# Kernel optimization log

Hardware: AMD Instinct MI355X
Metric: run time of the kernel (lower is better)

Reference implementation:

```python
import jax, jax.numpy as jnp
import numpy as np

N = 50000      # nodes
E = 500000     # edges (includes N self-loops)
DIN = 512
DOUT = 256
NEG_SLOPE = 0.01  # torch nn.LeakyReLU default


def setup_inputs() -> dict:
    key = jax.random.key(0)
    k1, k2, k3, k4, k5 = jax.random.split(key, 5)
    x = jax.random.normal(k1, (N, DIN), dtype=jnp.float32)
    # xavier_normal_ with gain=1.414
    std_W = 1.414 * np.sqrt(2.0 / (DIN + DOUT))
    W = jax.random.normal(k2, (DIN, DOUT), dtype=jnp.float32) * std_W
    std_a = 1.414 * np.sqrt(2.0 / (1 + 2 * DOUT))
    a = jax.random.normal(k3, (2 * DOUT,), dtype=jnp.float32) * std_a
    # first N edges are self-loops so every row-sum is nonzero
    loops = jnp.arange(N, dtype=jnp.int32)
    edge_src = jnp.concatenate([loops, jax.random.randint(k4, (E - N,), 0, N, dtype=jnp.int32)])
    edge_dst = jnp.concatenate([loops, jax.random.randint(k5, (E - N,), 0, N, dtype=jnp.int32)])
    return {"x": x, "W": W, "a": a, "edge_src": edge_src, "edge_dst": edge_dst}


def reference(x, W, a, edge_src, edge_dst):
    n = x.shape[0]
    d = W.shape[1]
    h = x @ W  # [N, DOUT]
    # a . [h_src ; h_dst] decomposed per-node, then gathered per-edge
    s_src = h @ a[:d]   # [N]
    s_dst = h @ a[d:]   # [N]
    score = s_src[edge_src] + s_dst[edge_dst]          # [E]
    e = jnp.exp(-jax.nn.leaky_relu(score, NEG_SLOPE))  # [E]
    # sparse softmax denominator: spmm(edge, e, ones) == segment sum over src
    e_rowsum = jax.ops.segment_sum(e, edge_src, num_segments=n)            # [N]
    # numerator: spmm(edge, e, h) == sum_j e_ij * h_j per row i
    h_prime = jax.ops.segment_sum(e[:, None] * h[edge_dst], edge_src, num_segments=n)  # [N, DOUT]
    h_prime = h_prime / e_rowsum[:, None]
    return jax.nn.elu(h_prime)  # concat=True branch
```

## Files before the change

### kernel.cpp

```cpp
#include <hip/hip_runtime.h>
#include <math.h>

#define DIN 512
#define DOUT 256
#define NEG_SLOPE 0.01f

typedef __attribute__((ext_vector_type(8))) short bf16x8;
typedef __attribute__((ext_vector_type(4))) float f32x4;
typedef __attribute__((ext_vector_type(4))) unsigned int u32x4;

__device__ __forceinline__ unsigned short f2bf(float f) {
    unsigned int u = __float_as_uint(f);
    unsigned int r = (u + 0x7FFFu + ((u >> 16) & 1u)) >> 16;
    return (unsigned short)r;
}
__device__ __forceinline__ float bf2f(unsigned short u) {
    return __uint_as_float(((unsigned int)u) << 16);
}
__device__ __forceinline__ unsigned int cvtpk(float lo, float hi) {
    unsigned int r;
    asm("v_cvt_pk_bf16_f32 %0, %1, %2" : "=v"(r) : "v"(lo), "v"(hi));
    return r;
}
__device__ __forceinline__ void gload16(const void* g, void* l) {
    __builtin_amdgcn_global_load_lds(
        (const __attribute__((address_space(1))) void*)g,
        (__attribute__((address_space(3))) void*)l, 16, 0, 0);
}

__global__ void prep(const float* __restrict__ W, unsigned short* __restrict__ Bp,
                     int* __restrict__ deg, float* __restrict__ s_src,
                     float* __restrict__ s_dst, int N) {
    int t = blockIdx.x * blockDim.x + threadIdx.x;
    if (t < (DIN / 32) * (DOUT / 16) * 64) {
        int lane = t & 63;
        int cg = (t >> 6) & 15;
        int ks = t >> 10;
        int l15 = lane & 15, g = lane >> 4;
        int col = cg * 16 + l15;
        int k0 = ks * 32 + g * 8;
        ushort4 lo, hi;
        lo.x = f2bf(W[(size_t)(k0 + 0) * DOUT + col]);
        lo.y = f2bf(W[(size_t)(k0 + 1) * DOUT + col]);
        lo.z = f2bf(W[(size_t)(k0 + 2) * DOUT + col]);
        lo.w = f2bf(W[(size_t)(k0 + 3) * DOUT + col]);
        hi.x = f2bf(W[(size_t)(k0 + 4) * DOUT + col]);
        hi.y = f2bf(W[(size_t)(k0 + 5) * DOUT + col]);
        hi.z = f2bf(W[(size_t)(k0 + 6) * DOUT + col]);
        hi.w = f2bf(W[(size_t)(k0 + 7) * DOUT + col]);
        *(ushort4*)(Bp + (size_t)t * 8) = lo;
        *(ushort4*)(Bp + (size_t)t * 8 + 4) = hi;
    }
    if (t < N) { deg[t] = 0; s_src[t] = 0.f; s_dst[t] = 0.f; }
}

__global__ __launch_bounds__(64, 3) void gemm_k(const float* __restrict__ x,
                                                const unsigned short* __restrict__ Bp,
                                                unsigned short* __restrict__ hb,
                                                const float* __restrict__ av,
                                                float* __restrict__ s_src,
                                                float* __restrict__ s_dst, int M) {
    __shared__ unsigned char As[16384];
    const int lane = threadIdx.x;
    const int l15 = lane & 15;
    const int g = lane >> 4;
    const int m0 = blockIdx.x * 32;
    const int half = blockIdx.y;

    auto stage = [&](int bb, int ks) {
#pragma unroll
        for (int it = 0; it < 4; ++it) {
            int s = it * 64 + lane;
            int row = s >> 3;
            int slot = s & 7;
            int q = slot ^ (row & 7);
            int rg = min(m0 + row, M - 1);
            const float* src = x + (size_t)rg * DIN + ks * 32 + q * 4;
            gload16(src, As + bb * 4096 + it * 1024);
        }
    };

    const unsigned short* pB = Bp + ((size_t)(half * 8) * 64 + lane) * 8;
    f32x4 acc[2][8] = {};
    bf16x8 bB[2][8];

    stage(0, 0);
    stage(1, 1);
#pragma unroll
    for (int cg = 0; cg < 8; ++cg)
        bB[0][cg] = *(const bf16x8*)(pB + (size_t)cg * 512);

#pragma unroll
    for (int ks = 0; ks < 16; ++ks) {
        if (ks < 14) stage((ks + 2) & 3, ks + 2);
        if (ks < 15) {
            const unsigned short* pBn = pB + (size_t)(ks + 1) * 16 * 512;
#pragma unroll
            for (int cg = 0; cg < 8; ++cg)
                bB[(ks + 1) & 1][cg] = *(const bf16x8*)(pBn + (size_t)cg * 512);
        }
        __builtin_amdgcn_sched_barrier(0);
        if (ks < 14)      asm volatile("s_waitcnt vmcnt(24)");
        else if (ks == 14) asm volatile("s_waitcnt vmcnt(20)");
        else               asm volatile("s_waitcnt vmcnt(16)");
        __builtin_amdgcn_sched_barrier(0);
        const unsigned char* Ab = As + (ks & 3) * 4096;
        const int rr0 = l15, rr1 = l15 + 16;
        f32x4 v0 = *(const f32x4*)(Ab + rr0 * 128 + (((2 * g) ^ (rr0 & 7)) << 4));
        f32x4 v1 = *(const f32x4*)(Ab + rr0 * 128 + (((2 * g + 1) ^ (rr0 & 7)) << 4));
        f32x4 w0 = *(const f32x4*)(Ab + rr1 * 128 + (((2 * g) ^ (rr1 & 7)) << 4));
        f32x4 w1 = *(const f32x4*)(Ab + rr1 * 128 + (((2 * g + 1) ^ (rr1 & 7)) << 4));
        u32x4 p;
        p.x = cvtpk(v0.x, v0.y); p.y = cvtpk(v0.z, v0.w);
        p.z = cvtpk(v1.x, v1.y); p.w = cvtpk(v1.z, v1.w);
        bf16x8 af0 = *(bf16x8*)&p;
        u32x4 q;
        q.x = cvtpk(w0.x, w0.y); q.y = cvtpk(w0.z, w0.w);
        q.z = cvtpk(w1.x, w1.y); q.w = cvtpk(w1.z, w1.w);
        bf16x8 af1 = *(bf16x8*)&q;
#pragma unroll
        for (int cg = 0; cg < 8; ++cg) {
            acc[0][cg] = __builtin_amdgcn_mfma_f32_16x16x32_bf16(af0, bB[ks & 1][cg], acc[0][cg], 0, 0, 0);
            acc[1][cg] = __builtin_amdgcn_mfma_f32_16x16x32_bf16(af1, bB[ks & 1][cg], acc[1][cg], 0, 0, 0);
        }
    }

    float as_[8], ad_[8];
#pragma unroll
    for (int cg = 0; cg < 8; ++cg) {
        int col = half * 128 + cg * 16 + l15;
        as_[cg] = av[col];
        ad_[cg] = av[DOUT + col];
    }
#pragma unroll
    for (int rf = 0; rf < 2; ++rf) {
#pragma unroll
        for (int j = 0; j < 4; ++j) {
            int row = m0 + rf * 16 + g * 4 + j;
            float ps = 0.f, pd = 0.f;
#pragma unroll
            for (int cg = 0; cg < 8; ++cg) {
                float v = acc[rf][cg][j];
                ps += v * as_[cg];
                pd += v * ad_[cg];
            }
#pragma unroll
            for (int off = 1; off < 16; off <<= 1) {
                ps += __shfl_xor(ps, off);
                pd += __shfl_xor(pd, off);
            }
            if (row < M) {
#pragma unroll
                for (int cg = 0; cg < 8; ++cg)
                    hb[(size_t)row * DOUT + half * 128 + cg * 16 + l15] = f2bf(acc[rf][cg][j]);
                if (l15 == 0) {
                    atomicAdd(&s_src[row], ps);
                    atomicAdd(&s_dst[row], pd);
                }
            }
        }
    }
}

__global__ void hist_k(const int* __restrict__ src, int* __restrict__ deg, int E) {
    int i = (blockIdx.x * blockDim.x + threadIdx.x) * 4;
    if (i + 3 < E) {
        int4 v = *(const int4*)(src + i);
        atomicAdd(&deg[v.x], 1);
        atomicAdd(&deg[v.y], 1);
        atomicAdd(&deg[v.z], 1);
        atomicAdd(&deg[v.w], 1);
    } else {
        for (int j = i; j < E; ++j) atomicAdd(&deg[src[j]], 1);
    }
}

__global__ __launch_bounds__(256) void block_sum(const int* __restrict__ deg, int* __restrict__ bsum, int N) {
    __shared__ int wsum[4];
    int b = blockIdx.x, t = threadIdx.x;
    int idx = b * 1024 + t * 4;
    int s = 0;
    if (idx + 3 < N) {
        int4 v = *(const int4*)(deg + idx);
        s = v.x + v.y + v.z + v.w;
    } else {
        for (int i = 0; i < 4; i++) if (idx + i < N) s += deg[idx + i];
    }
#pragma unroll
    for (int off = 32; off > 0; off >>= 1) s += __shfl_xor(s, off);
    if ((t & 63) == 0) wsum[t >> 6] = s;
    __syncthreads();
    if (t == 0) bsum[b] = wsum[0] + wsum[1] + wsum[2] + wsum[3];
}

__global__ __launch_bounds__(256) void scan_blk(const int* __restrict__ deg, const int* __restrict__ bsum,
                                                int* __restrict__ rowptr, int* __restrict__ cursor,
                                                int N, int nb, int E) {
    __shared__ int wsum[4];
    __shared__ int boff_s;
    int b = blockIdx.x, t = threadIdx.x;
    if (t < 64) {
        int v = (t < b && t < nb) ? bsum[t] : 0;
#pragma unroll
        for (int off = 32; off > 0; off >>= 1) v += __shfl_xor(v, off);
        if (t == 0) boff_s = v;
    }
    if (b == 0 && t == 0) rowptr[N] = E;
    int idx = b * 1024 + t * 4;
    int v0 = 0, v1 = 0, v2 = 0, v3 = 0;
    if (idx + 3 < N) {
        int4 v = *(const int4*)(deg + idx);
        v0 = v.x; v1 = v.y; v2 = v.z; v3 = v.w;
    } else if (idx < N) {
        v0 = deg[idx];
        if (idx + 1 < N) v1 = deg[idx + 1];
        if (idx + 2 < N) v2 = deg[idx + 2];
    }
    int s = v0 + v1 + v2 + v3;
    int lane = t & 63, wid = t >> 6;
    int x = s;
#pragma unroll
    for (int off = 1; off < 64; off <<= 1) {
        int y = __shfl_up(x, off);
        if (lane >= off) x += y;
    }
    if (lane == 63) wsum[wid] = x;
    __syncthreads();
    int add = boff_s;
    for (int ww = 0; ww < wid; ++ww) add += wsum[ww];
    int e0 = add + x - s;
    int e1 = e0 + v0, e2 = e1 + v1, e3 = e2 + v2;
    if (idx < N)     { rowptr[idx] = e0;     cursor[idx] = e0; }
    if (idx + 1 < N) { rowptr[idx + 1] = e1; cursor[idx + 1] = e1; }
    if (idx + 2 < N) { rowptr[idx + 2] = e2; cursor[idx + 2] = e2; }
    if (idx + 3 < N) { rowptr[idx + 3] = e3; cursor[idx + 3] = e3; }
}

__global__ void edge_k(const int* __restrict__ src, const int* __restrict__ dst,
                       const float* __restrict__ s_src, const float* __restrict__ s_dst,
                       int* __restrict__ cursor, int2* __restrict__ csr, int E) {
    int i = blockIdx.x * blockDim.x + threadIdx.x;
    if (i >= E) return;
    int s = src[i], d = dst[i];
    float sc = s_src[s] + s_dst[d];
    float lrv = sc > 0.f ? sc : NEG_SLOPE * sc;
    float ev = __expf(-lrv);
    int pos = atomicAdd(&cursor[s], 1);
    csr[pos] = make_int2(d, __float_as_int(ev));
}

__global__ __launch_bounds__(256) void gather_k(const unsigned short* __restrict__ hb,
                                                const int* __restrict__ rowptr,
                                                const int2* __restrict__ csr,
                                                float* __restrict__ out, int N) {
    int gt = blockIdx.x * blockDim.x + threadIdx.x;
    int w = gt >> 6;
    int lane = threadIdx.x & 63;
    if (w >= N) return;
    int s0 = rowptr[w], s1 = rowptr[w + 1];
    float a0 = 0.f, a1 = 0.f, a2 = 0.f, a3 = 0.f, rs = 0.f;
    for (int base = s0; base < s1; base += 64) {
        int cnt = min(64, s1 - base);
        int dv = 0; float ev = 0.f;
        if (lane < cnt) {
            int2 p = csr[base + lane];
            dv = p.x; ev = __int_as_float(p.y);
        }
        int jj = 0;
        for (; jj + 4 <= cnt; jj += 4) {
            int d0 = __shfl(dv, jj), d1 = __shfl(dv, jj + 1), d2 = __shfl(dv, jj + 2), d3 = __shfl(dv, jj + 3);
            float e0 = __shfl(ev, jj), e1 = __shfl(ev, jj + 1), e2 = __shfl(ev, jj + 2), e3 = __shfl(ev, jj + 3);
            ushort4 h0 = *(const ushort4*)(hb + (size_t)d0 * DOUT + lane * 4);
            ushort4 h1 = *(const ushort4*)(hb + (size_t)d1 * DOUT + lane * 4);
            ushort4 h2 = *(const ushort4*)(hb + (size_t)d2 * DOUT + lane * 4);
            ushort4 h3 = *(const ushort4*)(hb + (size_t)d3 * DOUT + lane * 4);
            a0 += e0 * bf2f(h0.x) + e1 * bf2f(h1.x) + e2 * bf2f(h2.x) + e3 * bf2f(h3.x);
            a1 += e0 * bf2f(h0.y) + e1 * bf2f(h1.y) + e2 * bf2f(h2.y) + e3 * bf2f(h3.y);
            a2 += e0 * bf2f(h0.z) + e1 * bf2f(h1.z) + e2 * bf2f(h2.z) + e3 * bf2f(h3.z);
            a3 += e0 * bf2f(h0.w) + e1 * bf2f(h1.w) + e2 * bf2f(h2.w) + e3 * bf2f(h3.w);
            rs += e0 + e1 + e2 + e3;
        }
        for (; jj < cnt; ++jj) {
            int d0 = __shfl(dv, jj);
            float e0 = __shfl(ev, jj);
            ushort4 h0 = *(const ushort4*)(hb + (size_t)d0 * DOUT + lane * 4);
            a0 += e0 * bf2f(h0.x);
            a1 += e0 * bf2f(h0.y);
            a2 += e0 * bf2f(h0.z);
            a3 += e0 * bf2f(h0.w);
            rs += e0;
        }
    }
    float inv = 1.f / rs;
    float4 v;
    v.x = a0 * inv; v.y = a1 * inv; v.z = a2 * inv; v.w = a3 * inv;
    v.x = v.x > 0.f ? v.x : __expf(v.x) - 1.f;
    v.y = v.y > 0.f ? v.y : __expf(v.y) - 1.f;
    v.z = v.z > 0.f ? v.z : __expf(v.z) - 1.f;
    v.w = v.w > 0.f ? v.w : __expf(v.w) - 1.f;
    *(float4*)(out + (size_t)w * DOUT + lane * 4) = v;
}

extern "C" void kernel_launch(void* const* d_in, const int* in_sizes, int n_in,
                              void* d_out, int out_size, void* d_ws, size_t ws_size,
                              hipStream_t stream) {
    const float* x = (const float*)d_in[0];
    const float* W = (const float*)d_in[1];
    const float* a = (const float*)d_in[2];
    const int* edge_src = (const int*)d_in[3];
    const int* edge_dst = (const int*)d_in[4];

    const int N = in_sizes[0] / DIN;
    const int E = in_sizes[3];
    const int nb = (N + 1023) / 1024;

    char* ws = (char*)d_ws;
    size_t off = 0;
    auto alloc = [&](size_t bytes) {
        void* p = ws + off;
        off += (bytes + 15) & ~(size_t)15;
        return p;
    };
    unsigned short* hb = (unsigned short*)alloc((size_t)N * DOUT * 2);
    unsigned short* Bp = (unsigned short*)alloc((size_t)DIN * DOUT * 2);
    int* rowptr = (int*)alloc((size_t)(N + 1) * 4);
    int* deg = (int*)alloc((size_t)N * 4);
    int* cursor = (int*)alloc((size_t)N * 4);
    float* s_src = (float*)alloc((size_t)N * 4);
    float* s_dst = (float*)alloc((size_t)N * 4);
    int2* csr = (int2*)alloc((size_t)E * 8);
    int* bsum = (int*)alloc((size_t)nb * 4);
    (void)ws_size;

    float* out = (float*)d_out;

    prep<<<(N + 255) / 256, 256, 0, stream>>>(W, Bp, deg, s_src, s_dst, N);
    hist_k<<<(E / 4 + 255) / 256, 256, 0, stream>>>(edge_src, deg, E);
    dim3 ggrid((N + 31) / 32, 2);
    gemm_k<<<ggrid, 64, 0, stream>>>(x, Bp, hb, a, s_src, s_dst, N);
    block_sum<<<nb, 256, 0, stream>>>(deg, bsum, N);
    scan_blk<<<nb, 256, 0, stream>>>(deg, bsum, rowptr, cursor, N, nb, E);
    edge_k<<<(E + 255) / 256, 256, 0, stream>>>(edge_src, edge_dst, s_src, s_dst,
                                                cursor, csr, E);
    gather_k<<<(N + 3) / 4, 256, 0, stream>>>(hb, rowptr, csr, out, N);
}
```

Baseline: 143.5 us.

## Fuse histogram into prep, move edge scoring into gather, simplify GEMM pipeline

The W-packing kernel now also builds the degree histogram, and the zeroing moves to a single memset. The edge kernel only scatters destination indices into the CSR, and edge scores and exponentials are computed inside the gather kernel. That halves the CSR footprint and lets the CSR build run before the GEMM. The GEMM drops from a 4-stage LDS ring with register-prefetched B to a 2-stage double buffer that loads B directly, trading latency hiding for lower LDS use. The gather kernel now splits each wavefront into two half-waves that load 16-byte rows of two edges at once and reduce across halves at the end.

```diff
diff --git a/kernel.cpp b/kernel.cpp
--- a/kernel.cpp
+++ b/kernel.cpp
@@ -14,9 +14,6 @@
     unsigned int r = (u + 0x7FFFu + ((u >> 16) & 1u)) >> 16;
     return (unsigned short)r;
 }
-__device__ __forceinline__ float bf2f(unsigned short u) {
-    return __uint_as_float(((unsigned int)u) << 16);
-}
 __device__ __forceinline__ unsigned int cvtpk(float lo, float hi) {
     unsigned int r;
     asm("v_cvt_pk_bf16_f32 %0, %1, %2" : "=v"(r) : "v"(lo), "v"(hi));
@@ -28,9 +25,8 @@
         (__attribute__((address_space(3))) void*)l, 16, 0, 0);
 }
 
-__global__ void prep(const float* __restrict__ W, unsigned short* __restrict__ Bp,
-                     int* __restrict__ deg, float* __restrict__ s_src,
-                     float* __restrict__ s_dst, int N) {
+__global__ void prep_hist(const float* __restrict__ W, unsigned short* __restrict__ Bp,
+                          const int* __restrict__ esrc, int* __restrict__ deg, int E) {
     int t = blockIdx.x * blockDim.x + threadIdx.x;
     if (t < (DIN / 32) * (DOUT / 16) * 64) {
         int lane = t & 63;
@@ -51,7 +47,16 @@
         *(ushort4*)(Bp + (size_t)t * 8) = lo;
         *(ushort4*)(Bp + (size_t)t * 8 + 4) = hi;
     }
-    if (t < N) { deg[t] = 0; s_src[t] = 0.f; s_dst[t] = 0.f; }
+    int i = t * 4;
+    if (i + 3 < E) {
+        int4 v = *(const int4*)(esrc + i);
+        atomicAdd(&deg[v.x], 1);
+        atomicAdd(&deg[v.y], 1);
+        atomicAdd(&deg[v.z], 1);
+        atomicAdd(&deg[v.w], 1);
+    } else {
+        for (int j = i; j < E; ++j) atomicAdd(&deg[esrc[j]], 1);
+    }
 }
 
 __global__ __launch_bounds__(64, 3) void gemm_k(const float* __restrict__ x,
@@ -60,7 +65,7 @@
                                                 const float* __restrict__ av,
                                                 float* __restrict__ s_src,
                                                 float* __restrict__ s_dst, int M) {
-    __shared__ unsigned char As[16384];
+    __shared__ unsigned char As[8192];
     const int lane = threadIdx.x;
     const int l15 = lane & 15;
     const int g = lane >> 4;
@@ -82,29 +87,18 @@
 
     const unsigned short* pB = Bp + ((size_t)(half * 8) * 64 + lane) * 8;
     f32x4 acc[2][8] = {};
-    bf16x8 bB[2][8];
 
     stage(0, 0);
-    stage(1, 1);
-#pragma unroll
-    for (int cg = 0; cg < 8; ++cg)
-        bB[0][cg] = *(const bf16x8*)(pB + (size_t)cg * 512);
-
 #pragma unroll
     for (int ks = 0; ks < 16; ++ks) {
-        if (ks < 14) stage((ks + 2) & 3, ks + 2);
+        const int bb = ks & 1;
         if (ks < 15) {
-            const unsigned short* pBn = pB + (size_t)(ks + 1) * 16 * 512;
-#pragma unroll
-            for (int cg = 0; cg < 8; ++cg)
-                bB[(ks + 1) & 1][cg] = *(const bf16x8*)(pBn + (size_t)cg * 512);
-        }
-        __builtin_amdgcn_sched_barrier(0);
-        if (ks < 14)      asm volatile("s_waitcnt vmcnt(24)");
-        else if (ks == 14) asm volatile("s_waitcnt vmcnt(20)");
-        else               asm volatile("s_waitcnt vmcnt(16)");
-        __builtin_amdgcn_sched_barrier(0);
-        const unsigned char* Ab = As + (ks & 3) * 4096;
+            stage(bb ^ 1, ks + 1);
+            asm volatile("s_waitcnt vmcnt(4)" ::: "memory");
+        } else {
+            asm volatile("s_waitcnt vmcnt(0)" ::: "memory");
+        }
+        const unsigned char* Ab = As + bb * 4096;
         const int rr0 = l15, rr1 = l15 + 16;
         f32x4 v0 = *(const f32x4*)(Ab + rr0 * 128 + (((2 * g) ^ (rr0 & 7)) << 4));
         f32x4 v1 = *(const f32x4*)(Ab + rr0 * 128 + (((2 * g + 1) ^ (rr0 & 7)) << 4));
@@ -118,10 +112,12 @@
         q.x = cvtpk(w0.x, w0.y); q.y = cvtpk(w0.z, w0.w);
         q.z = cvtpk(w1.x, w1.y); q.w = cvtpk(w1.z, w1.w);
         bf16x8 af1 = *(bf16x8*)&q;
+        const unsigned short* pBks = pB + (size_t)ks * 16 * 512;
 #pragma unroll
         for (int cg = 0; cg < 8; ++cg) {
-            acc[0][cg] = __builtin_amdgcn_mfma_f32_16x16x32_bf16(af0, bB[ks & 1][cg], acc[0][cg], 0, 0, 0);
-            acc[1][cg] = __builtin_amdgcn_mfma_f32_16x16x32_bf16(af1, bB[ks & 1][cg], acc[1][cg], 0, 0, 0);
+            bf16x8 bfr = *(const bf16x8*)(pBks + (size_t)cg * 512);
+            acc[0][cg] = __builtin_amdgcn_mfma_f32_16x16x32_bf16(af0, bfr, acc[0][cg], 0, 0, 0);
+            acc[1][cg] = __builtin_amdgcn_mfma_f32_16x16x32_bf16(af1, bfr, acc[1][cg], 0, 0, 0);
         }
     }
 
@@ -159,19 +155,6 @@
                 }
             }
         }
-    }
-}
-
-__global__ void hist_k(const int* __restrict__ src, int* __restrict__ deg, int E) {
-    int i = (blockIdx.x * blockDim.x + threadIdx.x) * 4;
-    if (i + 3 < E) {
-        int4 v = *(const int4*)(src + i);
-        atomicAdd(&deg[v.x], 1);
-        atomicAdd(&deg[v.y], 1);
-        atomicAdd(&deg[v.z], 1);
-        atomicAdd(&deg[v.w], 1);
-    } else {
-        for (int j = i; j < E; ++j) atomicAdd(&deg[src[j]], 1);
     }
 }
 
@@ -237,68 +220,110 @@
 }
 
 __global__ void edge_k(const int* __restrict__ src, const int* __restrict__ dst,
-                       const float* __restrict__ s_src, const float* __restrict__ s_dst,
-                       int* __restrict__ cursor, int2* __restrict__ csr, int E) {
+                       int* __restrict__ cursor, int* __restrict__ csr_d, int E) {
     int i = blockIdx.x * blockDim.x + threadIdx.x;
     if (i >= E) return;
-    int s = src[i], d = dst[i];
-    float sc = s_src[s] + s_dst[d];
-    float lrv = sc > 0.f ? sc : NEG_SLOPE * sc;
-    float ev = __expf(-lrv);
+    int s = src[i];
     int pos = atomicAdd(&cursor[s], 1);
-    csr[pos] = make_int2(d, __float_as_int(ev));
+    csr_d[pos] = dst[i];
 }
 
 __global__ __launch_bounds__(256) void gather_k(const unsigned short* __restrict__ hb,
                                                 const int* __restrict__ rowptr,
-                                                const int2* __restrict__ csr,
+                                                const int* __restrict__ csr_d,
+                                                const float* __restrict__ s_src,
+                                                const float* __restrict__ s_dst,
                                                 float* __restrict__ out, int N) {
     int gt = blockIdx.x * blockDim.x + threadIdx.x;
     int w = gt >> 6;
     int lane = threadIdx.x & 63;
     if (w >= N) return;
+    const int hl = lane & 31;
+    const int hf = lane >> 5;
     int s0 = rowptr[w], s1 = rowptr[w + 1];
-    float a0 = 0.f, a1 = 0.f, a2 = 0.f, a3 = 0.f, rs = 0.f;
+    float ss = s_src[w];
+    f32x4 acc0 = {0.f, 0.f, 0.f, 0.f}, acc1 = {0.f, 0.f, 0.f, 0.f};
+    float rs = 0.f;
+
     for (int base = s0; base < s1; base += 64) {
         int cnt = min(64, s1 - base);
         int dv = 0; float ev = 0.f;
         if (lane < cnt) {
-            int2 p = csr[base + lane];
-            dv = p.x; ev = __int_as_float(p.y);
+            dv = csr_d[base + lane];
+            float sc = ss + s_dst[dv];
+            float lr = sc > 0.f ? sc : NEG_SLOPE * sc;
+            ev = __expf(-lr);
         }
         int jj = 0;
-        for (; jj + 4 <= cnt; jj += 4) {
-            int d0 = __shfl(dv, jj), d1 = __shfl(dv, jj + 1), d2 = __shfl(dv, jj + 2), d3 = __shfl(dv, jj + 3);
-            float e0 = __shfl(ev, jj), e1 = __shfl(ev, jj + 1), e2 = __shfl(ev, jj + 2), e3 = __shfl(ev, jj + 3);
-            ushort4 h0 = *(const ushort4*)(hb + (size_t)d0 * DOUT + lane * 4);
-            ushort4 h1 = *(const ushort4*)(hb + (size_t)d1 * DOUT + lane * 4);
-            ushort4 h2 = *(const ushort4*)(hb + (size_t)d2 * DOUT + lane * 4);
-            ushort4 h3 = *(const ushort4*)(hb + (size_t)d3 * DOUT + lane * 4);
-            a0 += e0 * bf2f(h0.x) + e1 * bf2f(h1.x) + e2 * bf2f(h2.x) + e3 * bf2f(h3.x);
-            a1 += e0 * bf2f(h0.y) + e1 * bf2f(h1.y) + e2 * bf2f(h2.y) + e3 * bf2f(h3.y);
-            a2 += e0 * bf2f(h0.z) + e1 * bf2f(h1.z) + e2 * bf2f(h2.z) + e3 * bf2f(h3.z);
-            a3 += e0 * bf2f(h0.w) + e1 * bf2f(h1.w) + e2 * bf2f(h2.w) + e3 * bf2f(h3.w);
-            rs += e0 + e1 + e2 + e3;
-        }
-        for (; jj < cnt; ++jj) {
-            int d0 = __shfl(dv, jj);
-            float e0 = __shfl(ev, jj);
-            ushort4 h0 = *(const ushort4*)(hb + (size_t)d0 * DOUT + lane * 4);
-            a0 += e0 * bf2f(h0.x);
-            a1 += e0 * bf2f(h0.y);
-            a2 += e0 * bf2f(h0.z);
-            a3 += e0 * bf2f(h0.w);
-            rs += e0;
-        }
-    }
-    float inv = 1.f / rs;
-    float4 v;
-    v.x = a0 * inv; v.y = a1 * inv; v.z = a2 * inv; v.w = a3 * inv;
-    v.x = v.x > 0.f ? v.x : __expf(v.x) - 1.f;
-    v.y = v.y > 0.f ? v.y : __expf(v.y) - 1.f;
-    v.z = v.z > 0.f ? v.z : __expf(v.z) - 1.f;
-    v.w = v.w > 0.f ? v.w : __expf(v.w) - 1.f;
-    *(float4*)(out + (size_t)w * DOUT + lane * 4) = v;
+        for (; jj + 8 <= cnt; jj += 8) {
+            int dd[4]; float ee[4];
+#pragma unroll
+            for (int p = 0; p < 4; ++p) {
+                int idx = jj + 2 * p + hf;
+                dd[p] = __shfl(dv, idx);
+                ee[p] = __shfl(ev, idx);
+            }
+            u32x4 hv[4];
+#pragma unroll
+            for (int p = 0; p < 4; ++p)
+                hv[p] = *(const u32x4*)(hb + (size_t)dd[p] * DOUT + hl * 8);
+#pragma unroll
+            for (int p = 0; p < 4; ++p) {
+                float e = ee[p];
+                acc0.x += e * __uint_as_float(hv[p].x << 16);
+                acc0.y += e * __uint_as_float(hv[p].x & 0xffff0000u);
+                acc0.z += e * __uint_as_float(hv[p].y << 16);
+                acc0.w += e * __uint_as_float(hv[p].y & 0xffff0000u);
+                acc1.x += e * __uint_as_float(hv[p].z << 16);
+                acc1.y += e * __uint_as_float(hv[p].z & 0xffff0000u);
+                acc1.z += e * __uint_as_float(hv[p].w << 16);
+                acc1.w += e * __uint_as_float(hv[p].w & 0xffff0000u);
+                rs += e;
+            }
+        }
+        for (; jj < cnt; jj += 2) {
+            int idx = jj + hf;
+            int dd = __shfl(dv, idx & 63);
+            float e = __shfl(ev, idx & 63);
+            u32x4 hv = *(const u32x4*)(hb + (size_t)dd * DOUT + hl * 8);
+            acc0.x += e * __uint_as_float(hv.x << 16);
+            acc0.y += e * __uint_as_float(hv.x & 0xffff0000u);
+            acc0.z += e * __uint_as_float(hv.y << 16);
+            acc0.w += e * __uint_as_float(hv.y & 0xffff0000u);
+            acc1.x += e * __uint_as_float(hv.z << 16);
+            acc1.y += e * __uint_as_float(hv.z & 0xffff0000u);
+            acc1.z += e * __uint_as_float(hv.w << 16);
+            acc1.w += e * __uint_as_float(hv.w & 0xffff0000u);
+            rs += e;
+        }
+    }
+
+    rs += __shfl_xor(rs, 32);
+    acc0.x += __shfl_xor(acc0.x, 32);
+    acc0.y += __shfl_xor(acc0.y, 32);
+    acc0.z += __shfl_xor(acc0.z, 32);
+    acc0.w += __shfl_xor(acc0.w, 32);
+    acc1.x += __shfl_xor(acc1.x, 32);
+    acc1.y += __shfl_xor(acc1.y, 32);
+    acc1.z += __shfl_xor(acc1.z, 32);
+    acc1.w += __shfl_xor(acc1.w, 32);
+
+    if (hf == 0) {
+        float inv = 1.f / rs;
+        f32x4 r0, r1;
+        r0.x = acc0.x * inv; r0.y = acc0.y * inv; r0.z = acc0.z * inv; r0.w = acc0.w * inv;
+        r1.x = acc1.x * inv; r1.y = acc1.y * inv; r1.z = acc1.z * inv; r1.w = acc1.w * inv;
+        r0.x = r0.x > 0.f ? r0.x : __expf(r0.x) - 1.f;
+        r0.y = r0.y > 0.f ? r0.y : __expf(r0.y) - 1.f;
+        r0.z = r0.z > 0.f ? r0.z : __expf(r0.z) - 1.f;
+        r0.w = r0.w > 0.f ? r0.w : __expf(r0.w) - 1.f;
+        r1.x = r1.x > 0.f ? r1.x : __expf(r1.x) - 1.f;
+        r1.y = r1.y > 0.f ? r1.y : __expf(r1.y) - 1.f;
+        r1.z = r1.z > 0.f ? r1.z : __expf(r1.z) - 1.f;
+        r1.w = r1.w > 0.f ? r1.w : __expf(r1.w) - 1.f;
+        *(f32x4*)(out + (size_t)w * DOUT + hl * 8) = r0;
+        *(f32x4*)(out + (size_t)w * DOUT + hl * 8 + 4) = r1;
+    }
 }
 
 extern "C" void kernel_launch(void* const* d_in, const int* in_sizes, int n_in,
@@ -325,22 +350,22 @@
     unsigned short* Bp = (unsigned short*)alloc((size_t)DIN * DOUT * 2);
     int* rowptr = (int*)alloc((size_t)(N + 1) * 4);
     int* deg = (int*)alloc((size_t)N * 4);
-    int* cursor = (int*)alloc((size_t)N * 4);
     float* s_src = (float*)alloc((size_t)N * 4);
     float* s_dst = (float*)alloc((size_t)N * 4);
-    int2* csr = (int2*)alloc((size_t)E * 8);
+    int* cursor = (int*)alloc((size_t)N * 4);
+    int* csr_d = (int*)alloc((size_t)E * 4);
     int* bsum = (int*)alloc((size_t)nb * 4);
     (void)ws_size;
 
     float* out = (float*)d_out;
 
-    prep<<<(N + 255) / 256, 256, 0, stream>>>(W, Bp, deg, s_src, s_dst, N);
-    hist_k<<<(E / 4 + 255) / 256, 256, 0, stream>>>(edge_src, deg, E);
+    size_t zbytes = ((size_t)N * 4 + 15 & ~(size_t)15) * 2 + (size_t)N * 4;
+    hipMemsetAsync(deg, 0, zbytes, stream);
+    prep_hist<<<(E / 4 + 255) / 256, 256, 0, stream>>>(W, Bp, edge_src, deg, E);
+    block_sum<<<nb, 256, 0, stream>>>(deg, bsum, N);
+    scan_blk<<<nb, 256, 0, stream>>>(deg, bsum, rowptr, cursor, N, nb, E);
+    edge_k<<<(E + 255) / 256, 256, 0, stream>>>(edge_src, edge_dst, cursor, csr_d, E);
     dim3 ggrid((N + 31) / 32, 2);
     gemm_k<<<ggrid, 64, 0, stream>>>(x, Bp, hb, a, s_src, s_dst, N);
-    block_sum<<<nb, 256, 0, stream>>>(deg, bsum, N);
-    scan_blk<<<nb, 256, 0, stream>>>(deg, bsum, rowptr, cursor, N, nb, E);
-    edge_k<<<(E + 255) / 256, 256, 0, stream>>>(edge_src, edge_dst, s_src, s_dst,
-                                                cursor, csr, E);
-    gather_k<<<(N + 3) / 4, 256, 0, stream>>>(hb, rowptr, csr, out, N);
-}
+    gather_k<<<(N + 3) / 4, 256, 0, stream>>>(hb, rowptr, csr_d, s_src, s_dst, out, N);
+}
```

Measured after the change: 147.6 us. 1.03x slower.
